# Performance work log

Measured on AMD Instinct MI355X. Metric: run time of the kernel, lower is better.

## Reference

```python
import jax, jax.numpy as jnp
import numpy as np

_EPS = 1e-8
TEMPERATURE = 0.1  # head_cfg.temperature
WEIGHT = 1.0       # float(head_cfg.weight[1:]) with weight='w1'
N = 100000
K = 31   # nsample - 1
C = 64
NUM_CLASSES = 17


def setup_inputs() -> dict:
    key = jax.random.key(0)
    k1, k2, k3 = jax.random.split(key, 3)
    features = jax.random.normal(k1, (N, C), dtype=jnp.float32)
    labels = jax.random.randint(k2, (N,), 0, NUM_CLASSES, dtype=jnp.int32)
    # KNN neighbor indices with self excluded (original drops idx[...,1:]);
    # offset trick guarantees neighbor_idx[i, j] != i.
    off = jax.random.randint(k3, (N, K), 1, N, dtype=jnp.int32)
    neighbor_idx = (jnp.arange(N, dtype=jnp.int32)[:, None] + off) % N
    return {"features": features, "labels": labels, "neighbor_idx": neighbor_idx}


def reference(features, labels, neighbor_idx):
    # posmask_cnt: argmax of one-hot labels == integer class-id comparison
    neighbor_label = labels[neighbor_idx]                      # (N, K) int
    posmask = labels[:, None] == neighbor_label                # (N, K) bool
    cnt = posmask.sum(axis=1)
    point_mask = (cnt > 0) & (cnt < K)                          # (N,) bool

    # dist_l2 on gathered neighbor features
    neighbor_feature = features[neighbor_idx]                  # (N, K, C)
    diff = features[:, None, :] - neighbor_feature             # (N, K, C)
    dist = jnp.sqrt(jnp.sum(diff * diff, axis=-1)) + _EPS      # (N, K)

    # contrast_softnn
    logits = -dist
    logits = logits - jnp.max(logits, axis=1, keepdims=True)
    logits = logits / TEMPERATURE
    exp = jnp.exp(logits)                                      # (N, K)
    pos = jnp.sum(exp * posmask, axis=1)
    neg = jnp.sum(exp, axis=1)
    loss = -jnp.log(pos / neg + _EPS)                          # (N,)

    # masked mean == torch.mean(loss[point_mask])
    pm = point_mask.astype(loss.dtype)
    denom = jnp.maximum(jnp.sum(pm), 1.0)
    return jnp.sum(loss * pm) / denom * WEIGHT
```

## Files before the change

kernel.cpp:

```cpp
#include <hip/hip_runtime.h>
#include <hip/hip_fp16.h>

#define KNB 31
#define CH 64
#define TEMP_INV 10.0f

typedef _Float16 h2 __attribute__((ext_vector_type(2)));
typedef float f2 __attribute__((ext_vector_type(2)));


__global__ void ch_init_ws(double* __restrict__ ws) {
    ws[0] = 0.0;
    ws[1] = 0.0;
}

__global__ __launch_bounds__(256) void ch_cvt8(
    const float* __restrict__ in, unsigned char* __restrict__ out, int total8)
{
    const int idx = blockIdx.x * blockDim.x + threadIdx.x;
    if (idx >= total8) return;
    const float4* ip = reinterpret_cast<const float4*>(in) + (size_t)idx * 2;
    const float4 a = ip[0];
    const float4 b = ip[1];
    unsigned lo = 0u, hi = 0u;
    lo = __builtin_amdgcn_cvt_pk_fp8_f32(a.x, a.y, lo, false);
    lo = __builtin_amdgcn_cvt_pk_fp8_f32(a.z, a.w, lo, true);
    hi = __builtin_amdgcn_cvt_pk_fp8_f32(b.x, b.y, hi, false);
    hi = __builtin_amdgcn_cvt_pk_fp8_f32(b.z, b.w, hi, true);
    uint2 o; o.x = lo; o.y = hi;
    reinterpret_cast<uint2*>(out)[idx] = o;
}

__global__ __launch_bounds__(256) void ch_main8q(
    const unsigned char* __restrict__ tab8,
    const int*           __restrict__ labels,
    const int*           __restrict__ nidx,
    double*              __restrict__ ws,
    int n)
{
    const int t   = threadIdx.x;
    const int i   = blockIdx.x * (256 / 4) + (t >> 2);
    const int sub = t & 3;

    float loss_w = 0.0f;
    float pm_f   = 0.0f;

    if (i < n) {
        float fA[16];
        {
            union { uint4 u; unsigned w[4]; } Au;
            Au.u = reinterpret_cast<const uint4*>(tab8 + (size_t)i * CH)[sub];
            #pragma unroll
            for (int q = 0; q < 4; ++q) {
                const f2 p0 = __builtin_amdgcn_cvt_pk_f32_fp8(Au.w[q], false);
                const f2 p1 = __builtin_amdgcn_cvt_pk_f32_fp8(Au.w[q], true);
                fA[4 * q + 0] = p0[0]; fA[4 * q + 1] = p0[1];
                fA[4 * q + 2] = p1[0]; fA[4 * q + 3] = p1[1];
            }
        }

        const int lab = labels[i];
        const int* nrow = nidx + (size_t)i * KNB;

        float m  = -1e30f;
        float se = 0.0f;
        float sp = 0.0f;
        int   cnt = 0;

        #pragma unroll 4
        for (int j = 0; j < KNB; ++j) {
            const int nj = nrow[j];

            union { uint4 u; unsigned w[4]; } Bu;
            Bu.u = reinterpret_cast<const uint4*>(tab8 + (size_t)nj * CH)[sub];

            float s = 0.0f;
            #pragma unroll
            for (int q = 0; q < 4; ++q) {
                const f2 p0 = __builtin_amdgcn_cvt_pk_f32_fp8(Bu.w[q], false);
                const f2 p1 = __builtin_amdgcn_cvt_pk_f32_fp8(Bu.w[q], true);
                float d;
                d = fA[4 * q + 0] - p0[0]; s = fmaf(d, d, s);
                d = fA[4 * q + 1] - p0[1]; s = fmaf(d, d, s);
                d = fA[4 * q + 2] - p1[0]; s = fmaf(d, d, s);
                d = fA[4 * q + 3] - p1[1]; s = fmaf(d, d, s);
            }
            s += __shfl_xor(s, 1);
            s += __shfl_xor(s, 2);

            const float l = -(sqrtf(s) + 1e-8f);
            const bool pm = (labels[nj] == lab);
            cnt += pm ? 1 : 0;

            if (l > m) {
                const float r = __expf((m - l) * TEMP_INV);
                se *= r;
                sp *= r;
                m = l;
            }
            const float e = __expf((l - m) * TEMP_INV);
            se += e;
            if (pm) sp += e;
        }

        if (sub == 0 && cnt > 0 && cnt < KNB) {
            loss_w = -logf(sp / se + 1e-8f);
            pm_f   = 1.0f;
        }
    }

    __shared__ float s_l[256];
    __shared__ float s_c[256];
    s_l[t] = loss_w;
    s_c[t] = pm_f;
    __syncthreads();
    #pragma unroll
    for (int off = 128; off > 0; off >>= 1) {
        if (t < off) {
            s_l[t] += s_l[t + off];
            s_c[t] += s_c[t + off];
        }
        __syncthreads();
    }
    if (t == 0) {
        atomicAdd(ws,     (double)s_l[0]);
        atomicAdd(ws + 1, (double)s_c[0]);
    }
}

__global__ __launch_bounds__(256) void ch_cvt(
    const float* __restrict__ in, __half* __restrict__ out, int total8)
{
    const int idx = blockIdx.x * blockDim.x + threadIdx.x;
    if (idx >= total8) return;
    const float4* ip = reinterpret_cast<const float4*>(in) + (size_t)idx * 2;
    const float4 a = ip[0];
    const float4 b = ip[1];
    union { uint4 u; __half2 h[4]; } o;
    o.h[0] = __floats2half2_rn(a.x, a.y);
    o.h[1] = __floats2half2_rn(a.z, a.w);
    o.h[2] = __floats2half2_rn(b.x, b.y);
    o.h[3] = __floats2half2_rn(b.z, b.w);
    reinterpret_cast<uint4*>(out)[idx] = o.u;
}

__device__ __forceinline__ float dot2acc(h2 d, float s) {
    return __builtin_amdgcn_fdot2(d, d, s, false);
}

template <bool FP16>
__global__ __launch_bounds__(256) void ch_main4(
    const float*  __restrict__ feat,
    const __half* __restrict__ tab,
    const int*    __restrict__ labels,
    const int*    __restrict__ nidx,
    double*       __restrict__ ws,
    int n)
{
    const int t   = threadIdx.x;
    const int i   = blockIdx.x * (256 / 4) + (t >> 2);
    const int sub = t & 3;

    float loss_w = 0.0f;
    float pm_f   = 0.0f;

    if (i < n) {
        float f[16];
        union { uint4 u[2]; h2 h[8]; } A;
        if constexpr (FP16) {
            const uint4* ap = reinterpret_cast<const uint4*>(tab + (size_t)i * CH + sub * 16);
            A.u[0] = ap[0];
            A.u[1] = ap[1];
        } else {
            const float4* ap = reinterpret_cast<const float4*>(feat + (size_t)i * CH + sub * 16);
            #pragma unroll
            for (int q = 0; q < 4; ++q) {
                const float4 v = ap[q];
                f[4 * q]     = v.x;
                f[4 * q + 1] = v.y;
                f[4 * q + 2] = v.z;
                f[4 * q + 3] = v.w;
            }
        }

        const int lab = labels[i];

        float m  = -1e30f;
        float se = 0.0f;
        float sp = 0.0f;
        int   cnt = 0;

        #pragma unroll 2
        for (int j = 0; j < KNB; ++j) {
            const int nj = nidx[(size_t)i * KNB + j];

            float s = 0.0f;
            if constexpr (FP16) {
                union { uint4 u[2]; h2 h[8]; } B;
                const uint4* bp = reinterpret_cast<const uint4*>(tab + (size_t)nj * CH + sub * 16);
                B.u[0] = bp[0];
                B.u[1] = bp[1];
                #pragma unroll
                for (int q = 0; q < 8; ++q) {
                    const h2 d = A.h[q] - B.h[q];
                    s = dot2acc(d, s);
                }
            } else {
                const float4* bp = reinterpret_cast<const float4*>(feat + (size_t)nj * CH + sub * 16);
                #pragma unroll
                for (int q = 0; q < 4; ++q) {
                    const float4 v = bp[q];
                    const float dx = f[4 * q]     - v.x;
                    const float dy = f[4 * q + 1] - v.y;
                    const float dz = f[4 * q + 2] - v.z;
                    const float dw = f[4 * q + 3] - v.w;
                    s += dx * dx + dy * dy + dz * dz + dw * dw;
                }
            }
            s += __shfl_xor(s, 1);
            s += __shfl_xor(s, 2);

            const float dist = sqrtf(s) + 1e-8f;
            const float l = -dist;

            const bool pm = (labels[nj] == lab);
            cnt += pm ? 1 : 0;

            if (l > m) {
                const float r = __expf((m - l) * TEMP_INV);
                se *= r;
                sp *= r;
                m = l;
            }
            const float e = __expf((l - m) * TEMP_INV);
            se += e;
            if (pm) sp += e;
        }

        if (sub == 0 && cnt > 0 && cnt < KNB) {
            loss_w = -logf(sp / se + 1e-8f);
            pm_f   = 1.0f;
        }
    }

    __shared__ float s_l[256];
    __shared__ float s_c[256];
    s_l[t] = loss_w;
    s_c[t] = pm_f;
    __syncthreads();
    #pragma unroll
    for (int off = 128; off > 0; off >>= 1) {
        if (t < off) {
            s_l[t] += s_l[t + off];
            s_c[t] += s_c[t + off];
        }
        __syncthreads();
    }
    if (t == 0) {
        atomicAdd(ws,     (double)s_l[0]);
        atomicAdd(ws + 1, (double)s_c[0]);
    }
}

__global__ void ch_finalize(const double* __restrict__ ws, float* __restrict__ out) {
    double c = ws[1];
    if (c < 1.0) c = 1.0;
    out[0] = (float)(ws[0] / c);
}

extern "C" void kernel_launch(void* const* d_in, const int* in_sizes, int n_in,
                              void* d_out, int out_size, void* d_ws, size_t ws_size,
                              hipStream_t stream) {
    const float* feat   = (const float*)d_in[0];
    const int*   labels = (const int*)d_in[1];
    const int*   nidx   = (const int*)d_in[2];
    float*       out    = (float*)d_out;
    double*      ws     = (double*)d_ws;

    const int n = in_sizes[1];
    const int total8 = n * CH / 8;
    const int blocks = (n + 63) / 64;

    ch_init_ws<<<1, 1, 0, stream>>>(ws);

    if (ws_size >= 256 + (size_t)n * CH) {
        unsigned char* tab = (unsigned char*)d_ws + 256;
        ch_cvt8<<<(total8 + 255) / 256, 256, 0, stream>>>(feat, tab, total8);
        ch_main8q<<<blocks, 256, 0, stream>>>(tab, labels, nidx, ws, n);
    } else if (ws_size >= 256 + (size_t)n * CH * 2) {
        __half* tab = reinterpret_cast<__half*>((char*)d_ws + 256);
        ch_cvt<<<(total8 + 255) / 256, 256, 0, stream>>>(feat, tab, total8);
        ch_main4<true><<<blocks, 256, 0, stream>>>(feat, tab, labels, nidx, ws, n);
    } else {
        ch_main4<false><<<blocks, 256, 0, stream>>>(feat, nullptr, labels, nidx, ws, n);
    }

    ch_finalize<<<1, 1, 0, stream>>>(ws, out);
}
```

Measured before the change: 84.27 us.

## Process two points per quad and fold init/finalize into neighboring kernels

Each 4-lane group now handles two query points interleaved in the neighbor loop, so more independent gathers are in flight per thread. Workspace zeroing moves into the conversion kernel and finalization into the main kernel via a last-block atomic counter, which removes two tiny launches. The cost is more registers per thread and a grid-wide completion counter that is cleared only by thread 0 of the conversion kernel. There is also a latent validity issue: the outer guard checks only the first point.

```diff
diff --git a/kernel.cpp b/kernel.cpp
--- a/kernel.cpp
+++ b/kernel.cpp
@@ -9,15 +9,18 @@
 typedef float f2 __attribute__((ext_vector_type(2)));
 
 
-__global__ void ch_init_ws(double* __restrict__ ws) {
+__global__ void ch_init_ws(double* __restrict__ ws, unsigned* __restrict__ ctr) {
     ws[0] = 0.0;
     ws[1] = 0.0;
+    *ctr  = 0u;
 }
 
 __global__ __launch_bounds__(256) void ch_cvt8(
-    const float* __restrict__ in, unsigned char* __restrict__ out, int total8)
+    const float* __restrict__ in, unsigned char* __restrict__ out,
+    double* __restrict__ ws, unsigned* __restrict__ ctr, int total8)
 {
     const int idx = blockIdx.x * blockDim.x + threadIdx.x;
+    if (idx == 0) { ws[0] = 0.0; ws[1] = 0.0; *ctr = 0u; }
     if (idx >= total8) return;
     const float4* ip = reinterpret_cast<const float4*>(in) + (size_t)idx * 2;
     const float4 a = ip[0];
@@ -31,81 +34,116 @@
     reinterpret_cast<uint2*>(out)[idx] = o;
 }
 
-__global__ __launch_bounds__(256) void ch_main8q(
+__device__ __forceinline__ void fp8_to_f32x16(const uint4 u, float* f) {
+    union { uint4 v; unsigned w[4]; } U;
+    U.v = u;
+    #pragma unroll
+    for (int q = 0; q < 4; ++q) {
+        const f2 p0 = __builtin_amdgcn_cvt_pk_f32_fp8(U.w[q], false);
+        const f2 p1 = __builtin_amdgcn_cvt_pk_f32_fp8(U.w[q], true);
+        f[4 * q + 0] = p0[0]; f[4 * q + 1] = p0[1];
+        f[4 * q + 2] = p1[0]; f[4 * q + 3] = p1[1];
+    }
+}
+
+__global__ __launch_bounds__(256, 4) void ch_main8q2(
     const unsigned char* __restrict__ tab8,
     const int*           __restrict__ labels,
     const int*           __restrict__ nidx,
     double*              __restrict__ ws,
+    unsigned*            __restrict__ ctr,
+    float*               __restrict__ out,
     int n)
 {
-    const int t   = threadIdx.x;
-    const int i   = blockIdx.x * (256 / 4) + (t >> 2);
-    const int sub = t & 3;
+    const int t    = threadIdx.x;
+    const int qid  = t >> 2;
+    const int sub  = t & 3;
+    const int i0   = blockIdx.x * 128 + qid;
+    const int i1   = i0 + 64;
+    const bool v0  = (i0 < n);
+    const bool v1  = (i1 < n);
+    const int i0c  = v0 ? i0 : 0;
+    const int i1c  = v1 ? i1 : 0;
 
     float loss_w = 0.0f;
     float pm_f   = 0.0f;
 
-    if (i < n) {
-        float fA[16];
-        {
-            union { uint4 u; unsigned w[4]; } Au;
-            Au.u = reinterpret_cast<const uint4*>(tab8 + (size_t)i * CH)[sub];
+    if (v0) {
+        float fA0[16], fA1[16];
+        fp8_to_f32x16(reinterpret_cast<const uint4*>(tab8 + (size_t)i0c * CH)[sub], fA0);
+        fp8_to_f32x16(reinterpret_cast<const uint4*>(tab8 + (size_t)i1c * CH)[sub], fA1);
+
+        const int lab0 = labels[i0c];
+        const int lab1 = labels[i1c];
+        const int* nrow0 = nidx + (size_t)i0c * KNB;
+        const int* nrow1 = nidx + (size_t)i1c * KNB;
+
+        float m0 = -1e30f, se0 = 0.0f, sp0 = 0.0f;
+        float m1 = -1e30f, se1 = 0.0f, sp1 = 0.0f;
+        int cnt0 = 0, cnt1 = 0;
+
+        #pragma unroll 2
+        for (int j = 0; j < KNB; ++j) {
+            const int nj0 = nrow0[j];
+            const int nj1 = nrow1[j];
+
+            const uint4 b0 = reinterpret_cast<const uint4*>(tab8 + (size_t)nj0 * CH)[sub];
+            const uint4 b1 = reinterpret_cast<const uint4*>(tab8 + (size_t)nj1 * CH)[sub];
+
+            float fB[16];
+            float s0 = 0.0f, s1 = 0.0f;
+            fp8_to_f32x16(b0, fB);
             #pragma unroll
-            for (int q = 0; q < 4; ++q) {
-                const f2 p0 = __builtin_amdgcn_cvt_pk_f32_fp8(Au.w[q], false);
-                const f2 p1 = __builtin_amdgcn_cvt_pk_f32_fp8(Au.w[q], true);
-                fA[4 * q + 0] = p0[0]; fA[4 * q + 1] = p0[1];
-                fA[4 * q + 2] = p1[0]; fA[4 * q + 3] = p1[1];
-            }
-        }
-
-        const int lab = labels[i];
-        const int* nrow = nidx + (size_t)i * KNB;
-
-        float m  = -1e30f;
-        float se = 0.0f;
-        float sp = 0.0f;
-        int   cnt = 0;
-
-        #pragma unroll 4
-        for (int j = 0; j < KNB; ++j) {
-            const int nj = nrow[j];
-
-            union { uint4 u; unsigned w[4]; } Bu;
-            Bu.u = reinterpret_cast<const uint4*>(tab8 + (size_t)nj * CH)[sub];
-
-            float s = 0.0f;
+            for (int q = 0; q < 16; ++q) {
+                const float d = fA0[q] - fB[q];
+                s0 = fmaf(d, d, s0);
+            }
+            fp8_to_f32x16(b1, fB);
             #pragma unroll
-            for (int q = 0; q < 4; ++q) {
-                const f2 p0 = __builtin_amdgcn_cvt_pk_f32_fp8(Bu.w[q], false);
-                const f2 p1 = __builtin_amdgcn_cvt_pk_f32_fp8(Bu.w[q], true);
-                float d;
-                d = fA[4 * q + 0] - p0[0]; s = fmaf(d, d, s);
-                d = fA[4 * q + 1] - p0[1]; s = fmaf(d, d, s);
-                d = fA[4 * q + 2] - p1[0]; s = fmaf(d, d, s);
-                d = fA[4 * q + 3] - p1[1]; s = fmaf(d, d, s);
-            }
-            s += __shfl_xor(s, 1);
-            s += __shfl_xor(s, 2);
-
-            const float l = -(sqrtf(s) + 1e-8f);
-            const bool pm = (labels[nj] == lab);
-            cnt += pm ? 1 : 0;
-
-            if (l > m) {
-                const float r = __expf((m - l) * TEMP_INV);
-                se *= r;
-                sp *= r;
-                m = l;
-            }
-            const float e = __expf((l - m) * TEMP_INV);
-            se += e;
-            if (pm) sp += e;
-        }
-
-        if (sub == 0 && cnt > 0 && cnt < KNB) {
-            loss_w = -logf(sp / se + 1e-8f);
-            pm_f   = 1.0f;
+            for (int q = 0; q < 16; ++q) {
+                const float d = fA1[q] - fB[q];
+                s1 = fmaf(d, d, s1);
+            }
+
+            s0 += __shfl_xor(s0, 1);
+            s0 += __shfl_xor(s0, 2);
+            s1 += __shfl_xor(s1, 1);
+            s1 += __shfl_xor(s1, 2);
+
+            const float l0 = -(sqrtf(s0) + 1e-8f);
+            const float l1 = -(sqrtf(s1) + 1e-8f);
+
+            const bool pm0 = (labels[nj0] == lab0);
+            const bool pm1 = (labels[nj1] == lab1);
+            cnt0 += pm0 ? 1 : 0;
+            cnt1 += pm1 ? 1 : 0;
+
+            if (l0 > m0) {
+                const float r = __expf((m0 - l0) * TEMP_INV);
+                se0 *= r; sp0 *= r; m0 = l0;
+            }
+            const float e0 = __expf((l0 - m0) * TEMP_INV);
+            se0 += e0;
+            if (pm0) sp0 += e0;
+
+            if (l1 > m1) {
+                const float r = __expf((m1 - l1) * TEMP_INV);
+                se1 *= r; sp1 *= r; m1 = l1;
+            }
+            const float e1 = __expf((l1 - m1) * TEMP_INV);
+            se1 += e1;
+            if (pm1) sp1 += e1;
+        }
+
+        if (sub == 0) {
+            if (v0 && cnt0 > 0 && cnt0 < KNB) {
+                loss_w += -logf(sp0 / se0 + 1e-8f);
+                pm_f   += 1.0f;
+            }
+            if (v1 && cnt1 > 0 && cnt1 < KNB) {
+                loss_w += -logf(sp1 / se1 + 1e-8f);
+                pm_f   += 1.0f;
+            }
         }
     }
 
@@ -125,6 +163,14 @@
     if (t == 0) {
         atomicAdd(ws,     (double)s_l[0]);
         atomicAdd(ws + 1, (double)s_c[0]);
+        __threadfence();
+        const unsigned old = atomicAdd(ctr, 1u);
+        if (old == gridDim.x - 1) {
+            const double sl = atomicAdd(ws, 0.0);
+            const double sc = atomicAdd(ws + 1, 0.0);
+            const double c  = (sc < 1.0) ? 1.0 : sc;
+            out[0] = (float)(sl / c);
+        }
     }
 }
 
@@ -184,11 +230,8 @@
         }
 
         const int lab = labels[i];
-
-        float m  = -1e30f;
-        float se = 0.0f;
-        float sp = 0.0f;
-        int   cnt = 0;
+        float m = -1e30f, se = 0.0f, sp = 0.0f;
+        int cnt = 0;
 
         #pragma unroll 2
         for (int j = 0; j < KNB; ++j) {
@@ -220,17 +263,13 @@
             s += __shfl_xor(s, 1);
             s += __shfl_xor(s, 2);
 
-            const float dist = sqrtf(s) + 1e-8f;
-            const float l = -dist;
-
+            const float l = -(sqrtf(s) + 1e-8f);
             const bool pm = (labels[nj] == lab);
             cnt += pm ? 1 : 0;
 
             if (l > m) {
                 const float r = __expf((m - l) * TEMP_INV);
-                se *= r;
-                sp *= r;
-                m = l;
+                se *= r; sp *= r; m = l;
             }
             const float e = __expf((l - m) * TEMP_INV);
             se += e;
@@ -276,24 +315,27 @@
     const int*   nidx   = (const int*)d_in[2];
     float*       out    = (float*)d_out;
     double*      ws     = (double*)d_ws;
+    unsigned*    ctr    = (unsigned*)((char*)d_ws + 16);
 
     const int n = in_sizes[1];
     const int total8 = n * CH / 8;
-    const int blocks = (n + 63) / 64;
-
-    ch_init_ws<<<1, 1, 0, stream>>>(ws);
 
     if (ws_size >= 256 + (size_t)n * CH) {
         unsigned char* tab = (unsigned char*)d_ws + 256;
-        ch_cvt8<<<(total8 + 255) / 256, 256, 0, stream>>>(feat, tab, total8);
-        ch_main8q<<<blocks, 256, 0, stream>>>(tab, labels, nidx, ws, n);
-    } else if (ws_size >= 256 + (size_t)n * CH * 2) {
+        ch_cvt8<<<(total8 + 255) / 256, 256, 0, stream>>>(feat, tab, ws, ctr, total8);
+        const int blocks = (n + 127) / 128;
+        ch_main8q2<<<blocks, 256, 0, stream>>>(tab, labels, nidx, ws, ctr, out, n);
+        return;
+    }
+
+    ch_init_ws<<<1, 1, 0, stream>>>(ws, ctr);
+    const int blocks = (n + 63) / 64;
+    if (ws_size >= 256 + (size_t)n * CH * 2) {
         __half* tab = reinterpret_cast<__half*>((char*)d_ws + 256);
         ch_cvt<<<(total8 + 255) / 256, 256, 0, stream>>>(feat, tab, total8);
         ch_main4<true><<<blocks, 256, 0, stream>>>(feat, tab, labels, nidx, ws, n);
     } else {
         ch_main4<false><<<blocks, 256, 0, stream>>>(feat, nullptr, labels, nidx, ws, n);
     }
-
     ch_finalize<<<1, 1, 0, stream>>>(ws, out);
 }
```

Result: slower. 150.1 us (+78.2%).
